# Kernel optimization log

Hardware: AMD Instinct MI355X
Metric: run time of the kernel (lower is better)

Reference implementation:

```python
import jax, jax.numpy as jnp
import numpy as np

N = 50000      # nodes
NIN = 512      # input feature dim
H = 512        # hidden width (cfg[0])
D = 128        # output embedding (cfg[1])
A = 3          # number of adjacency matrices
E = 800000     # edges per adjacency (avg degree 16)
P_DROP = 0.2


def setup_inputs() -> dict:
    key = jax.random.key(0)
    ks = jax.random.split(key, 8)
    seq_a = jax.random.normal(ks[0], (N, NIN), jnp.float32)
    # xavier-uniform-ish scaling for linear layers
    W1 = jax.random.normal(ks[1], (NIN, H), jnp.float32) * (1.0 / np.sqrt(NIN))
    b1 = jnp.zeros((H,), jnp.float32)
    W2 = jax.random.normal(ks[2], (H, D), jnp.float32) * (1.0 / np.sqrt(H))
    b2 = jnp.zeros((D,), jnp.float32)
    # COO sparse adjacencies: A matrices, E edges each; vals ~ normalized weights
    rows = jax.random.randint(ks[3], (A, E), 0, N, jnp.int32)
    cols = jax.random.randint(ks[4], (A, E), 0, N, jnp.int32)
    vals = jax.random.uniform(ks[5], (A, E), jnp.float32) * (1.0 / 16.0)
    return {"seq_a": seq_a, "W1": W1, "b1": b1, "W2": W2, "b2": b2,
            "vals": vals, "rows": rows, "cols": cols}


def _dropout(x, key, p):
    keep = jax.random.bernoulli(key, 1.0 - p, x.shape)
    return jnp.where(keep, x / (1.0 - p), jnp.zeros((), x.dtype))


def _spmm(rows_i, cols_i, vals_i, h):
    # (sparse [N,N]) @ h  via gather + segment-sum
    msg = vals_i[:, None] * h[cols_i]           # [E, D]
    return jax.ops.segment_sum(msg, rows_i, num_segments=N)


def reference(seq_a, W1, b1, W2, b2, vals, rows, cols):
    key = jax.random.key(42)
    k0, k1 = jax.random.split(key)
    # input dropout -> 2-layer MLP (Linear, ReLU, Linear)
    x = _dropout(seq_a, k0, P_DROP)
    h = jax.nn.relu(x @ W1 + b1)
    h_a = h @ W2 + b2                            # [N, D]
    h_p_0 = _dropout(h_a, k1, P_DROP)
    # per-adjacency spmm (small fixed loop over A adjacencies)
    h_p_stack = jnp.stack(
        [_spmm(rows[i], cols[i], vals[i], h_p_0) for i in range(A)])  # [A, N, D]
    h_p_fusion = jnp.mean(h_p_stack, axis=0)     # [N, D]
    return (h_a, h_p_stack, h_p_fusion)
```

## Files before the change

### kernel.cpp

```cpp
#include <hip/hip_runtime.h>
#include <stdint.h>

#define N_NODES 50000
#define M_PAD   50048
#define NIN     512
#define HDIM    512
#define DDIM    128
#define A_ADJ   3
#define E_EDGES 800000
#define TOT_E   (A_ADJ * E_EDGES)
#define TOT_ROWS (A_ADJ * N_NODES)
#define CB      49
#define NB      (A_ADJ * CB)
#define CHUNK   2048
#define NCHB    ((TOT_E + CHUNK - 1) / CHUNK)
#define TRB     640
#define DIB     25000

typedef __bf16 bf16x8 __attribute__((ext_vector_type(8)));
typedef float  f32x4  __attribute__((ext_vector_type(4)));
typedef const __attribute__((address_space(1))) void* gas1_t;
typedef __attribute__((address_space(3))) void* las3_t;

__host__ __device__ inline void tf_round(uint32_t& x0, uint32_t& x1, int r) {
  x0 += x1; x1 = (x1 << r) | (x1 >> (32 - r)); x1 ^= x0;
}
__host__ __device__ inline void threefry2x32(uint32_t k0, uint32_t k1,
                                             uint32_t x0, uint32_t x1,
                                             uint32_t& o0, uint32_t& o1) {
  uint32_t ks2 = k0 ^ k1 ^ 0x1BD11BDAu;
  x0 += k0; x1 += k1;
  tf_round(x0,x1,13); tf_round(x0,x1,15); tf_round(x0,x1,26); tf_round(x0,x1,6);
  x0 += k1; x1 += ks2 + 1u;
  tf_round(x0,x1,17); tf_round(x0,x1,29); tf_round(x0,x1,16); tf_round(x0,x1,24);
  x0 += ks2; x1 += k0 + 2u;
  tf_round(x0,x1,13); tf_round(x0,x1,15); tf_round(x0,x1,26); tf_round(x0,x1,6);
  x0 += k0; x1 += k1 + 3u;
  tf_round(x0,x1,17); tf_round(x0,x1,29); tf_round(x0,x1,16); tf_round(x0,x1,24);
  x0 += k1; x1 += ks2 + 4u;
  tf_round(x0,x1,13); tf_round(x0,x1,15); tf_round(x0,x1,26); tf_round(x0,x1,6);
  x0 += ks2; x1 += k0 + 5u;
  o0 = x0; o1 = x1;
}

__device__ inline bool keep_bit(uint32_t b) {
  float f = __uint_as_float((b >> 9) | 0x3f800000u) - 1.0f;
  return f < 0.8f;
}
__device__ inline uint16_t f2bf(float f) {
  uint32_t u = __float_as_uint(f);
  return (uint16_t)((u + 0x7fffu + ((u >> 16) & 1u)) >> 16);
}
__device__ inline float bf2f(uint16_t b) { return __uint_as_float(((uint32_t)b) << 16); }

__device__ inline uint32_t rbits32(uint32_t ka, uint32_t kb, uint32_t i) {
  uint32_t o0, o1;
  threefry2x32(ka, kb, 0u, i, o0, o1);
  return o0 ^ o1;
}

template <int MODE>
__device__ __forceinline__ void gemm_body(const uint16_t* __restrict__ A,
                                          const uint16_t* __restrict__ Bt,
                                          const float* __restrict__ bias,
                                          uint16_t* __restrict__ hOut,
                                          float* __restrict__ fOut,
                                          uint16_t* __restrict__ hp0,
                                          int Nn, int K, int bx, int by,
                                          char* smem, uint32_t ka, uint32_t kb) {
  uint16_t* As0 = (uint16_t*)smem;
  uint16_t* Bs0 = As0 + 8192;
  const int t  = threadIdx.x;
  const int w  = t >> 6, l = t & 63;
  const int lm = l & 15, kg = l >> 4;
  const int wr = w >> 1, wc = w & 1;
  const int rowbase = by * 128;
  const int colbase = bx * 128;
  const int c0 = t, c1 = t + 256;
  const int n0 = c0 >> 2, ch0 = (c0 & 3) ^ ((n0 >> 1) & 3);
  const int n1 = c1 >> 2, ch1 = (c1 & 3) ^ ((n1 >> 1) & 3);

  f32x4 acc[4][4] = {};

#define STAGEB(buf, kt)                                                             \
  {                                                                                 \
    __builtin_amdgcn_global_load_lds(                                               \
        (gas1_t)&A [(size_t)(rowbase + n0) * K + (kt) + ch0 * 8],                   \
        (las3_t)(As0 + (buf) * 4096 + c0 * 8), 16, 0, 0);                           \
    __builtin_amdgcn_global_load_lds(                                               \
        (gas1_t)&A [(size_t)(rowbase + n1) * K + (kt) + ch1 * 8],                   \
        (las3_t)(As0 + (buf) * 4096 + c1 * 8), 16, 0, 0);                           \
    __builtin_amdgcn_global_load_lds(                                               \
        (gas1_t)&Bt[(size_t)(colbase + n0) * K + (kt) + ch0 * 8],                   \
        (las3_t)(Bs0 + (buf) * 4096 + c0 * 8), 16, 0, 0);                           \
    __builtin_amdgcn_global_load_lds(                                               \
        (gas1_t)&Bt[(size_t)(colbase + n1) * K + (kt) + ch1 * 8],                   \
        (las3_t)(Bs0 + (buf) * 4096 + c1 * 8), 16, 0, 0);                           \
  }

  STAGEB(0, 0);
  asm volatile("s_waitcnt vmcnt(0)" ::: "memory");
  __syncthreads();

  const int NT = K >> 5;
  for (int tt = 0; tt < NT; ++tt) {
    const int cur = tt & 1;
    if (tt + 1 < NT) STAGEB(cur ^ 1, (tt + 1) * 32);

    const uint16_t* Asc = As0 + cur * 4096;
    const uint16_t* Bsc = Bs0 + cur * 4096;
    bf16x8 af[4], bfr[4];
#pragma unroll
    for (int m = 0; m < 4; ++m) {
      int ra = wr * 64 + m * 16 + lm;
      af[m] = *(const bf16x8*)&Asc[ra * 32 + ((kg ^ ((ra >> 1) & 3)) << 3)];
    }
#pragma unroll
    for (int n = 0; n < 4; ++n) {
      int rb = wc * 64 + n * 16 + lm;
      bfr[n] = *(const bf16x8*)&Bsc[rb * 32 + ((kg ^ ((rb >> 1) & 3)) << 3)];
    }
#pragma unroll
    for (int m = 0; m < 4; ++m)
#pragma unroll
      for (int n = 0; n < 4; ++n)
        acc[m][n] = __builtin_amdgcn_mfma_f32_16x16x32_bf16(af[m], bfr[n], acc[m][n], 0, 0, 0);

    asm volatile("s_waitcnt vmcnt(0)" ::: "memory");
    __syncthreads();
  }
#undef STAGEB

#pragma unroll
  for (int m = 0; m < 4; ++m) {
    int r0 = rowbase + wr * 64 + m * 16 + kg * 4;
#pragma unroll
    for (int n = 0; n < 4; ++n) {
      int cc = colbase + wc * 64 + n * 16 + lm;
      float bv = bias[cc];
#pragma unroll
      for (int r = 0; r < 4; ++r) {
        int row = r0 + r;
        if (row < N_NODES) {
          float v = acc[m][n][r] + bv;
          if (MODE == 0) {
            hOut[(size_t)row * Nn + cc] = f2bf(fmaxf(v, 0.0f));
          } else {
            fOut[(size_t)row * Nn + cc] = v;
            uint32_t bits = rbits32(ka, kb, (uint32_t)(row * DDIM + cc));
            hp0[(size_t)row * DDIM + cc] = f2bf(keep_bit(bits) ? v * 1.25f : 0.0f);
          }
        }
      }
    }
  }
}

struct P1S {
  uint64_t lbuf[CHUNK];
  uint16_t lbkt[CHUNK];
  uint32_t hist[NB], scn[NB], lofs[NB], base[NB];
  uint32_t hs[256];
};

__device__ __forceinline__ void pass1_body(const int* __restrict__ rows,
                                           const int* __restrict__ cols,
                                           const float* __restrict__ vals,
                                           uint32_t* __restrict__ gcur,
                                           uint64_t* __restrict__ sedgeA,
                                           int blk, char* smem) {
  P1S* S = (P1S*)smem;
  const int tid = threadIdx.x;
  const int cb = blk * CHUNK;
  const int cnt = min(CHUNK, TOT_E - cb);

  if (tid < NB) S->hist[tid] = 0;
  __syncthreads();

  uint64_t pay[8];
  uint16_t bk[8];
#pragma unroll
  for (int c = 0; c < 8; ++c) {
    int p = tid + c * 256;
    bk[c] = 0xffffu;
    if (p < cnt) {
      int e = cb + p;
      int a = e / E_EDGES;
      uint32_t r   = (uint32_t)rows[e];
      uint32_t col = (uint32_t)cols[e];
      float    v   = vals[e];
      uint16_t b = (uint16_t)(a * CB + (r >> 10));
      pay[c] = ((uint64_t)__float_as_uint(v) << 32) | ((r & 1023u) << 16) | col;
      bk[c]  = b;
      atomicAdd(&S->hist[b], 1u);
    }
  }
  __syncthreads();

  uint32_t hv = (tid < NB) ? S->hist[tid] : 0u;
  S->hs[tid] = hv;
  __syncthreads();
  for (int off = 1; off < 256; off <<= 1) {
    uint32_t v = (tid >= off) ? S->hs[tid - off] : 0u;
    __syncthreads();
    S->hs[tid] += v;
    __syncthreads();
  }
  if (tid < NB) {
    uint32_t excl = S->hs[tid] - hv;
    S->scn[tid]  = excl;
    S->lofs[tid] = excl;
    S->base[tid] = hv ? atomicAdd(&gcur[tid], hv) : 0u;
  }
  __syncthreads();

#pragma unroll
  for (int c = 0; c < 8; ++c) {
    if (bk[c] != 0xffffu) {
      uint32_t p = atomicAdd(&S->lofs[bk[c]], 1u);
      S->lbuf[p] = pay[c];
      S->lbkt[p] = bk[c];
    }
  }
  __syncthreads();

#pragma unroll
  for (int c = 0; c < 8; ++c) {
    int p = tid + c * 256;
    if (p < cnt) {
      uint16_t k = S->lbkt[p];
      sedgeA[S->base[k] + ((uint32_t)p - S->scn[k])] = S->lbuf[p];
    }
  }
}

struct P2S { uint32_t rh[1024], rs[1024], wsum[256]; };

__device__ __forceinline__ void pass2_body(const uint32_t* __restrict__ gbase,
                                           const uint64_t* __restrict__ sedgeA,
                                           uint64_t* __restrict__ sedgeB,
                                           uint32_t* __restrict__ offs,
                                           int b, char* smem) {
  P2S* S = (P2S*)smem;
  const int tid = threadIdx.x;
  const int a = b / CB, rb = (b % CB) * 1024;
  const int nrows = min(1024, N_NODES - rb);
  const uint32_t s0 = gbase[b], e0 = gbase[b + 1];

#pragma unroll
  for (int c = 0; c < 4; ++c) S->rh[tid + c * 256] = 0;
  __syncthreads();
  for (uint32_t i = s0 + tid; i < e0; i += 256) {
    uint32_t rl = ((uint32_t)(sedgeA[i] >> 16)) & 1023u;
    atomicAdd(&S->rh[rl], 1u);
  }
  __syncthreads();

  uint32_t c0 = S->rh[tid * 4], c1 = S->rh[tid * 4 + 1];
  uint32_t c2 = S->rh[tid * 4 + 2], c3 = S->rh[tid * 4 + 3];
  uint32_t tsum = c0 + c1 + c2 + c3;
  S->wsum[tid] = tsum;
  __syncthreads();
  for (int off = 1; off < 256; off <<= 1) {
    uint32_t v = (tid >= off) ? S->wsum[tid - off] : 0u;
    __syncthreads();
    S->wsum[tid] += v;
    __syncthreads();
  }
  uint32_t run = S->wsum[tid] - tsum;
  S->rs[tid * 4] = run;     run += c0;
  S->rs[tid * 4 + 1] = run; run += c1;
  S->rs[tid * 4 + 2] = run; run += c2;
  S->rs[tid * 4 + 3] = run;
  __syncthreads();

  for (int r = tid; r < 1024; r += 256) {
    if (r < nrows) offs[(size_t)a * N_NODES + rb + r] = s0 + S->rs[r];
    S->rh[r] = S->rs[r];
  }
  __syncthreads();

  for (uint32_t i = s0 + tid; i < e0; i += 256) {
    uint64_t ed = sedgeA[i];
    uint32_t rl = ((uint32_t)(ed >> 16)) & 1023u;
    uint32_t p = atomicAdd(&S->rh[rl], 1u);
    sedgeB[s0 + p] = ed;
  }
}

__global__ __launch_bounds__(256) void k_front(const float* __restrict__ W1,
                                               uint16_t* __restrict__ w1t,
                                               const float* __restrict__ W2,
                                               uint16_t* __restrict__ w2t,
                                               const float* __restrict__ seq,
                                               uint16_t* __restrict__ x,
                                               const int* __restrict__ rows,
                                               uint32_t* __restrict__ gh,
                                               uint32_t ka, uint32_t kb) {
  __shared__ uint32_t shh[NB];
  const int b = blockIdx.x, tid = threadIdx.x;
  if (b < TRB) {
    int t = b * 256 + tid;
    const int T1 = (NIN * HDIM) / 2;
    if (t < T1) {
      int k2 = (2 * t) % NIN, n = (2 * t) / NIN;
      uint32_t p = (uint32_t)f2bf(W1[(size_t)k2 * HDIM + n])
                 | ((uint32_t)f2bf(W1[(size_t)(k2 + 1) * HDIM + n]) << 16);
      *(uint32_t*)&w1t[(size_t)n * NIN + k2] = p;
    } else {
      int u = t - T1;
      int k2 = (2 * u) % HDIM, n = (2 * u) / HDIM;
      uint32_t p = (uint32_t)f2bf(W2[(size_t)k2 * DDIM + n])
                 | ((uint32_t)f2bf(W2[(size_t)(k2 + 1) * DDIM + n]) << 16);
      *(uint32_t*)&w2t[(size_t)n * HDIM + k2] = p;
    }
  } else if (b < TRB + NCHB) {
    if (tid < NB) shh[tid] = 0;
    __syncthreads();
    const int cb = (b - TRB) * CHUNK;
    const int cnt = min(CHUNK, TOT_E - cb);
    for (int c = tid; c < cnt; c += 256) {
      int e = cb + c;
      int a = e / E_EDGES;
      uint32_t r = (uint32_t)rows[e];
      atomicAdd(&shh[a * CB + (r >> 10)], 1u);
    }
    __syncthreads();
    if (tid < NB && shh[tid]) atomicAdd(&gh[tid], shh[tid]);
  } else {
    int t = (b - TRB - NCHB) * 256 + tid;
    int i0 = 4 * t;
    float4 v = ((const float4*)seq)[t];
    float f[4] = {v.x, v.y, v.z, v.w};
    uint16_t r[4];
#pragma unroll
    for (int j = 0; j < 4; ++j) {
      uint32_t bits = rbits32(ka, kb, (uint32_t)(i0 + j));
      r[j] = f2bf(keep_bit(bits) ? f[j] * 1.25f : 0.0f);
    }
    uint2 w;
    w.x = (uint32_t)r[0] | ((uint32_t)r[1] << 16);
    w.y = (uint32_t)r[2] | ((uint32_t)r[3] << 16);
    ((uint2*)x)[t] = w;
  }
}

__global__ __launch_bounds__(256) void k_bscan(const uint32_t* __restrict__ gh,
                                               uint32_t* __restrict__ gbase,
                                               uint32_t* __restrict__ gcur,
                                               uint32_t* __restrict__ offs) {
  __shared__ uint32_t s[256];
  const int tid = threadIdx.x;
  uint32_t v = (tid < NB) ? gh[tid] : 0u;
  s[tid] = v;
  __syncthreads();
  for (int off = 1; off < 256; off <<= 1) {
    uint32_t w = (tid >= off) ? s[tid - off] : 0u;
    __syncthreads();
    s[tid] += w;
    __syncthreads();
  }
  if (tid < NB) { uint32_t excl = s[tid] - v; gbase[tid] = excl; gcur[tid] = excl; }
  if (tid == NB - 1) gbase[NB] = s[tid];
  if (tid == 0) offs[TOT_ROWS] = (uint32_t)TOT_E;
}

__global__ __launch_bounds__(256) void k_mid(const uint16_t* __restrict__ x,
                                             const uint16_t* __restrict__ w1t,
                                             const float* __restrict__ b1,
                                             uint16_t* __restrict__ h,
                                             const int* __restrict__ rows,
                                             const int* __restrict__ cols,
                                             const float* __restrict__ vals,
                                             uint32_t* __restrict__ gcur,
                                             uint64_t* __restrict__ sedgeA) {
  __shared__ __align__(16) char smem[32768];
  const int b = blockIdx.x;
  if (b < 4 * (M_PAD / 128))
    gemm_body<0>(x, w1t, b1, h, nullptr, nullptr, HDIM, NIN, b & 3, b >> 2, smem, 0u, 0u);
  else
    pass1_body(rows, cols, vals, gcur, sedgeA, b - 4 * (M_PAD / 128), smem);
}

__global__ __launch_bounds__(256) void k_back(const uint16_t* __restrict__ h,
                                              const uint16_t* __restrict__ w2t,
                                              const float* __restrict__ b2,
                                              float* __restrict__ ha,
                                              uint16_t* __restrict__ hp0,
                                              const uint32_t* __restrict__ gbase,
                                              const uint64_t* __restrict__ sedgeA,
                                              uint64_t* __restrict__ sedgeB,
                                              uint32_t* __restrict__ offs,
                                              uint32_t ka, uint32_t kb) {
  __shared__ __align__(16) char smem[32768];
  const int b = blockIdx.x;
  if (b < M_PAD / 128)
    gemm_body<1>(h, w2t, b2, nullptr, ha, hp0, DDIM, HDIM, 0, b, smem, ka, kb);
  else
    pass2_body(gbase, sedgeA, sedgeB, offs, b - M_PAD / 128, smem);
}

__global__ __launch_bounds__(256) void k_spmm_csr3(const uint32_t* __restrict__ offs,
                                                   const uint64_t* __restrict__ sedge,
                                                   const uint16_t* __restrict__ hp0,
                                                   float* __restrict__ stack,
                                                   float* __restrict__ fus) {
  int row = (int)((blockIdx.x * (size_t)blockDim.x + threadIdx.x) >> 6);
  int l = threadIdx.x & 63;
  if (row >= N_NODES) return;
  const int q = l & 15, g = l >> 4;
  const uint4* hp4 = (const uint4*)hp0;
  float fs[8] = {};

#pragma unroll
  for (int a = 0; a < A_ADJ; ++a) {
    uint32_t s = offs[(size_t)a * N_NODES + row];
    uint32_t e = offs[(size_t)a * N_NODES + row + 1];
    float acc[8] = {};
    for (uint32_t i = s; i < e; i += 8) {
      uint32_t i0 = i + g, i1 = i + 4 + g;
      float v0 = 0.f, v1 = 0.f;
      uint32_t col0 = 0, col1 = 0;
      if (i0 < e) { uint64_t ed = sedge[i0]; col0 = (uint32_t)ed & 0xffffu;
                    v0 = __uint_as_float((uint32_t)(ed >> 32)); }
      if (i1 < e) { uint64_t ed = sedge[i1]; col1 = (uint32_t)ed & 0xffffu;
                    v1 = __uint_as_float((uint32_t)(ed >> 32)); }
      uint4 p0 = hp4[(size_t)col0 * 16 + q];
      uint4 p1 = hp4[(size_t)col1 * 16 + q];
      acc[0] += bf2f((uint16_t)(p0.x & 0xffffu)) * v0;  acc[1] += bf2f((uint16_t)(p0.x >> 16)) * v0;
      acc[2] += bf2f((uint16_t)(p0.y & 0xffffu)) * v0;  acc[3] += bf2f((uint16_t)(p0.y >> 16)) * v0;
      acc[4] += bf2f((uint16_t)(p0.z & 0xffffu)) * v0;  acc[5] += bf2f((uint16_t)(p0.z >> 16)) * v0;
      acc[6] += bf2f((uint16_t)(p0.w & 0xffffu)) * v0;  acc[7] += bf2f((uint16_t)(p0.w >> 16)) * v0;
      acc[0] += bf2f((uint16_t)(p1.x & 0xffffu)) * v1;  acc[1] += bf2f((uint16_t)(p1.x >> 16)) * v1;
      acc[2] += bf2f((uint16_t)(p1.y & 0xffffu)) * v1;  acc[3] += bf2f((uint16_t)(p1.y >> 16)) * v1;
      acc[4] += bf2f((uint16_t)(p1.z & 0xffffu)) * v1;  acc[5] += bf2f((uint16_t)(p1.z >> 16)) * v1;
      acc[6] += bf2f((uint16_t)(p1.w & 0xffffu)) * v1;  acc[7] += bf2f((uint16_t)(p1.w >> 16)) * v1;
    }
#pragma unroll
    for (int d = 0; d < 8; ++d) {
      acc[d] += __shfl_xor(acc[d], 16);
      acc[d] += __shfl_xor(acc[d], 32);
    }
    if (l < 16) {
      size_t b4 = ((size_t)a * N_NODES + row) * 32 + (size_t)q * 2;
      ((float4*)stack)[b4]     = make_float4(acc[0], acc[1], acc[2], acc[3]);
      ((float4*)stack)[b4 + 1] = make_float4(acc[4], acc[5], acc[6], acc[7]);
    }
#pragma unroll
    for (int d = 0; d < 8; ++d) fs[d] += acc[d];
  }
  if (l < 16) {
    const float k3 = 1.0f / 3.0f;
    size_t b4 = (size_t)row * 32 + (size_t)q * 2;
    ((float4*)fus)[b4]     = make_float4(fs[0] * k3, fs[1] * k3, fs[2] * k3, fs[3] * k3);
    ((float4*)fus)[b4 + 1] = make_float4(fs[4] * k3, fs[5] * k3, fs[6] * k3, fs[7] * k3);
  }
}

extern "C" void kernel_launch(void* const* d_in, const int* in_sizes, int n_in,
                              void* d_out, int out_size, void* d_ws, size_t ws_size,
                              hipStream_t stream) {
  const float* seq  = (const float*)d_in[0];
  const float* W1   = (const float*)d_in[1];
  const float* b1   = (const float*)d_in[2];
  const float* W2   = (const float*)d_in[3];
  const float* b2   = (const float*)d_in[4];
  const float* vals = (const float*)d_in[5];
  const int*   rows = (const int*)d_in[6];
  const int*   cols = (const int*)d_in[7];

  float* out       = (float*)d_out;
  float* out_ha    = out;
  float* out_stack = out + (size_t)N_NODES * DDIM;
  float* out_fus   = out_stack + (size_t)A_ADJ * N_NODES * DDIM;

  uint16_t* x   = (uint16_t*)d_ws;
  uint16_t* h   = x   + (size_t)M_PAD * NIN;
  uint16_t* w1t = h   + (size_t)M_PAD * HDIM;
  uint16_t* w2t = w1t + (size_t)HDIM * NIN;
  uint16_t* hp0 = w2t + (size_t)DDIM * HDIM;
  uint32_t* gh    = (uint32_t*)(hp0 + (size_t)N_NODES * DDIM);
  uint32_t* gbase = gh + 256;
  uint32_t* gcur  = gbase + 256;
  uint32_t* offs  = gcur + 256;

  uint64_t* sedgeA = (uint64_t*)out_stack;
  uint64_t* sedgeB = (uint64_t*)x;

  uint32_t k0a, k0b, k1a, k1b;
  threefry2x32(0u, 42u, 0u, 0u, k0a, k0b);
  threefry2x32(0u, 42u, 0u, 1u, k1a, k1b);

  (void)hipMemsetAsync(gh, 0, NB * sizeof(uint32_t), stream);

  k_front<<<TRB + NCHB + DIB, 256, 0, stream>>>(W1, w1t, W2, w2t, seq, x, rows, gh, k0a, k0b);

  k_bscan<<<1, 256, 0, stream>>>(gh, gbase, gcur, offs);

  k_mid<<<4 * (M_PAD / 128) + NCHB, 256, 0, stream>>>(x, w1t, b1, h, rows, cols, vals,
                                                      gcur, sedgeA);

  k_back<<<(M_PAD / 128) + NB, 256, 0, stream>>>(h, w2t, b2, out_ha, hp0,
                                                 gbase, sedgeA, sedgeB, offs, k1a, k1b);

  k_spmm_csr3<<<(N_NODES * 64 + 255) / 256, 256, 0, stream>>>(offs, sedgeB, hp0,
                                                              out_stack, out_fus);
}
```

Before: 294.2 us.

## Retile first GEMM as 64x512 full-width tiles with 512-thread blocks

The first GEMM (x @ W1) changes from 128x128 tiles over four column blocks to 64-row tiles that span the full 512-wide hidden dimension, with 8 waves per block. Each A tile is now loaded from global memory once instead of four times. The cost is more W1 traffic per block, 72KB of LDS and fewer blocks resident per CU. The co-scheduled edge-bucketing pass and k_mid are moved to 512 threads to match, and the spmm gather uses 32-bit byte offsets instead of 64-bit index math.

```diff
diff --git a/kernel.cpp b/kernel.cpp
--- a/kernel.cpp
+++ b/kernel.cpp
@@ -16,6 +16,7 @@
 #define NCHB    ((TOT_E + CHUNK - 1) / CHUNK)
 #define TRB     640
 #define DIB     25000
+#define G0B     (M_PAD / 64)
 
 typedef __bf16 bf16x8 __attribute__((ext_vector_type(8)));
 typedef float  f32x4  __attribute__((ext_vector_type(4)));
@@ -59,15 +60,88 @@
   return o0 ^ o1;
 }
 
-template <int MODE>
-__device__ __forceinline__ void gemm_body(const uint16_t* __restrict__ A,
-                                          const uint16_t* __restrict__ Bt,
-                                          const float* __restrict__ bias,
-                                          uint16_t* __restrict__ hOut,
-                                          float* __restrict__ fOut,
-                                          uint16_t* __restrict__ hp0,
-                                          int Nn, int K, int bx, int by,
-                                          char* smem, uint32_t ka, uint32_t kb) {
+__device__ __forceinline__ void gemm0_body(const uint16_t* __restrict__ x,
+                                           const uint16_t* __restrict__ w1t,
+                                           const float* __restrict__ b1,
+                                           uint16_t* __restrict__ h,
+                                           int by, char* smem) {
+  uint16_t* As0 = (uint16_t*)smem;
+  uint16_t* Bs0 = As0 + 2 * 2048;
+  const int tid = threadIdx.x;
+  const int l = tid & 63, wid = tid >> 6;
+  const int lm = l & 15, kg = l >> 4;
+  const int wrow = wid >> 2, wcol = wid & 3;
+  const int rowbase = by * 64;
+
+  f32x4 acc[2][8] = {};
+
+#define STAGE0(buf, kt)                                                             \
+  {                                                                                 \
+    if (tid < 256) {                                                                \
+      int row = tid >> 2, cs = tid & 3, ch = cs ^ ((row >> 1) & 3);                 \
+      __builtin_amdgcn_global_load_lds(                                             \
+          (gas1_t)&x[(size_t)(rowbase + row) * NIN + (kt) + ch * 8],                \
+          (las3_t)(As0 + (buf) * 2048 + tid * 8), 16, 0, 0);                        \
+    }                                                                               \
+    _Pragma("unroll")                                                               \
+    for (int it = 0; it < 4; ++it) {                                                \
+      int q = it * 512 + tid;                                                       \
+      int n = q >> 2, cs = q & 3, ch = cs ^ ((n >> 1) & 3);                         \
+      __builtin_amdgcn_global_load_lds(                                             \
+          (gas1_t)&w1t[(size_t)n * NIN + (kt) + ch * 8],                            \
+          (las3_t)(Bs0 + (buf) * 16384 + q * 8), 16, 0, 0);                         \
+    }                                                                               \
+  }
+
+  STAGE0(0, 0);
+  asm volatile("s_waitcnt vmcnt(0)" ::: "memory");
+  __syncthreads();
+
+  for (int tt = 0; tt < 16; ++tt) {
+    const int cur = tt & 1;
+    if (tt + 1 < 16) STAGE0(cur ^ 1, (tt + 1) * 32);
+
+    const uint16_t* Asc = As0 + cur * 2048;
+    const uint16_t* Bsc = Bs0 + cur * 16384;
+    const int r0a = wrow * 32 + lm, r1a = r0a + 16;
+    bf16x8 af0 = *(const bf16x8*)&Asc[r0a * 32 + ((kg ^ ((r0a >> 1) & 3)) << 3)];
+    bf16x8 af1 = *(const bf16x8*)&Asc[r1a * 32 + ((kg ^ ((r1a >> 1) & 3)) << 3)];
+#pragma unroll
+    for (int n = 0; n < 8; ++n) {
+      int rb = wcol * 128 + n * 16 + lm;
+      bf16x8 bfr = *(const bf16x8*)&Bsc[rb * 32 + ((kg ^ ((rb >> 1) & 3)) << 3)];
+      acc[0][n] = __builtin_amdgcn_mfma_f32_16x16x32_bf16(af0, bfr, acc[0][n], 0, 0, 0);
+      acc[1][n] = __builtin_amdgcn_mfma_f32_16x16x32_bf16(af1, bfr, acc[1][n], 0, 0, 0);
+    }
+    asm volatile("s_waitcnt vmcnt(0)" ::: "memory");
+    __syncthreads();
+  }
+#undef STAGE0
+
+#pragma unroll
+  for (int m = 0; m < 2; ++m) {
+    int r0 = rowbase + wrow * 32 + m * 16 + kg * 4;
+#pragma unroll
+    for (int n = 0; n < 8; ++n) {
+      int cc = wcol * 128 + n * 16 + lm;
+      float bv = b1[cc];
+#pragma unroll
+      for (int r = 0; r < 4; ++r) {
+        int row = r0 + r;
+        if (row < N_NODES)
+          h[(size_t)row * HDIM + cc] = f2bf(fmaxf(acc[m][n][r] + bv, 0.0f));
+      }
+    }
+  }
+}
+
+__device__ __forceinline__ void gemm1_body(const uint16_t* __restrict__ A,
+                                           const uint16_t* __restrict__ Bt,
+                                           const float* __restrict__ bias,
+                                           float* __restrict__ fOut,
+                                           uint16_t* __restrict__ hp0,
+                                           int by, char* smem,
+                                           uint32_t ka, uint32_t kb) {
   uint16_t* As0 = (uint16_t*)smem;
   uint16_t* Bs0 = As0 + 8192;
   const int t  = threadIdx.x;
@@ -75,14 +149,14 @@
   const int lm = l & 15, kg = l >> 4;
   const int wr = w >> 1, wc = w & 1;
   const int rowbase = by * 128;
-  const int colbase = bx * 128;
   const int c0 = t, c1 = t + 256;
   const int n0 = c0 >> 2, ch0 = (c0 & 3) ^ ((n0 >> 1) & 3);
   const int n1 = c1 >> 2, ch1 = (c1 & 3) ^ ((n1 >> 1) & 3);
+  const int K = HDIM;
 
   f32x4 acc[4][4] = {};
 
-#define STAGEB(buf, kt)                                                             \
+#define STAGE1(buf, kt)                                                             \
   {                                                                                 \
     __builtin_amdgcn_global_load_lds(                                               \
         (gas1_t)&A [(size_t)(rowbase + n0) * K + (kt) + ch0 * 8],                   \
@@ -91,21 +165,21 @@
         (gas1_t)&A [(size_t)(rowbase + n1) * K + (kt) + ch1 * 8],                   \
         (las3_t)(As0 + (buf) * 4096 + c1 * 8), 16, 0, 0);                           \
     __builtin_amdgcn_global_load_lds(                                               \
-        (gas1_t)&Bt[(size_t)(colbase + n0) * K + (kt) + ch0 * 8],                   \
+        (gas1_t)&Bt[(size_t)n0 * K + (kt) + ch0 * 8],                               \
         (las3_t)(Bs0 + (buf) * 4096 + c0 * 8), 16, 0, 0);                           \
     __builtin_amdgcn_global_load_lds(                                               \
-        (gas1_t)&Bt[(size_t)(colbase + n1) * K + (kt) + ch1 * 8],                   \
+        (gas1_t)&Bt[(size_t)n1 * K + (kt) + ch1 * 8],                               \
         (las3_t)(Bs0 + (buf) * 4096 + c1 * 8), 16, 0, 0);                           \
   }
 
-  STAGEB(0, 0);
+  STAGE1(0, 0);
   asm volatile("s_waitcnt vmcnt(0)" ::: "memory");
   __syncthreads();
 
   const int NT = K >> 5;
   for (int tt = 0; tt < NT; ++tt) {
     const int cur = tt & 1;
-    if (tt + 1 < NT) STAGEB(cur ^ 1, (tt + 1) * 32);
+    if (tt + 1 < NT) STAGE1(cur ^ 1, (tt + 1) * 32);
 
     const uint16_t* Asc = As0 + cur * 4096;
     const uint16_t* Bsc = Bs0 + cur * 4096;
@@ -129,27 +203,23 @@
     asm volatile("s_waitcnt vmcnt(0)" ::: "memory");
     __syncthreads();
   }
-#undef STAGEB
+#undef STAGE1
 
 #pragma unroll
   for (int m = 0; m < 4; ++m) {
     int r0 = rowbase + wr * 64 + m * 16 + kg * 4;
 #pragma unroll
     for (int n = 0; n < 4; ++n) {
-      int cc = colbase + wc * 64 + n * 16 + lm;
+      int cc = wc * 64 + n * 16 + lm;
       float bv = bias[cc];
 #pragma unroll
       for (int r = 0; r < 4; ++r) {
         int row = r0 + r;
         if (row < N_NODES) {
           float v = acc[m][n][r] + bv;
-          if (MODE == 0) {
-            hOut[(size_t)row * Nn + cc] = f2bf(fmaxf(v, 0.0f));
-          } else {
-            fOut[(size_t)row * Nn + cc] = v;
-            uint32_t bits = rbits32(ka, kb, (uint32_t)(row * DDIM + cc));
-            hp0[(size_t)row * DDIM + cc] = f2bf(keep_bit(bits) ? v * 1.25f : 0.0f);
-          }
+          fOut[(size_t)row * DDIM + cc] = v;
+          uint32_t bits = rbits32(ka, kb, (uint32_t)(row * DDIM + cc));
+          hp0[(size_t)row * DDIM + cc] = f2bf(keep_bit(bits) ? v * 1.25f : 0.0f);
         }
       }
     }
@@ -160,7 +230,7 @@
   uint64_t lbuf[CHUNK];
   uint16_t lbkt[CHUNK];
   uint32_t hist[NB], scn[NB], lofs[NB], base[NB];
-  uint32_t hs[256];
+  uint32_t hs[512];
 };
 
 __device__ __forceinline__ void pass1_body(const int* __restrict__ rows,
@@ -177,11 +247,11 @@
   if (tid < NB) S->hist[tid] = 0;
   __syncthreads();
 
-  uint64_t pay[8];
-  uint16_t bk[8];
-#pragma unroll
-  for (int c = 0; c < 8; ++c) {
-    int p = tid + c * 256;
+  uint64_t pay[4];
+  uint16_t bk[4];
+#pragma unroll
+  for (int c = 0; c < 4; ++c) {
+    int p = tid + c * 512;
     bk[c] = 0xffffu;
     if (p < cnt) {
       int e = cb + p;
@@ -200,7 +270,7 @@
   uint32_t hv = (tid < NB) ? S->hist[tid] : 0u;
   S->hs[tid] = hv;
   __syncthreads();
-  for (int off = 1; off < 256; off <<= 1) {
+  for (int off = 1; off < 512; off <<= 1) {
     uint32_t v = (tid >= off) ? S->hs[tid - off] : 0u;
     __syncthreads();
     S->hs[tid] += v;
@@ -215,7 +285,7 @@
   __syncthreads();
 
 #pragma unroll
-  for (int c = 0; c < 8; ++c) {
+  for (int c = 0; c < 4; ++c) {
     if (bk[c] != 0xffffu) {
       uint32_t p = atomicAdd(&S->lofs[bk[c]], 1u);
       S->lbuf[p] = pay[c];
@@ -225,8 +295,8 @@
   __syncthreads();
 
 #pragma unroll
-  for (int c = 0; c < 8; ++c) {
-    int p = tid + c * 256;
+  for (int c = 0; c < 4; ++c) {
+    int p = tid + c * 512;
     if (p < cnt) {
       uint16_t k = S->lbkt[p];
       sedgeA[S->base[k] + ((uint32_t)p - S->scn[k])] = S->lbuf[p];
@@ -365,7 +435,7 @@
   if (tid == 0) offs[TOT_ROWS] = (uint32_t)TOT_E;
 }
 
-__global__ __launch_bounds__(256) void k_mid(const uint16_t* __restrict__ x,
+__global__ __launch_bounds__(512) void k_mid(const uint16_t* __restrict__ x,
                                              const uint16_t* __restrict__ w1t,
                                              const float* __restrict__ b1,
                                              uint16_t* __restrict__ h,
@@ -374,12 +444,12 @@
                                              const float* __restrict__ vals,
                                              uint32_t* __restrict__ gcur,
                                              uint64_t* __restrict__ sedgeA) {
-  __shared__ __align__(16) char smem[32768];
+  __shared__ __align__(16) char smem[73728];
   const int b = blockIdx.x;
-  if (b < 4 * (M_PAD / 128))
-    gemm_body<0>(x, w1t, b1, h, nullptr, nullptr, HDIM, NIN, b & 3, b >> 2, smem, 0u, 0u);
+  if (b < G0B)
+    gemm0_body(x, w1t, b1, h, b, smem);
   else
-    pass1_body(rows, cols, vals, gcur, sedgeA, b - 4 * (M_PAD / 128), smem);
+    pass1_body(rows, cols, vals, gcur, sedgeA, b - G0B, smem);
 }
 
 __global__ __launch_bounds__(256) void k_back(const uint16_t* __restrict__ h,
@@ -395,7 +465,7 @@
   __shared__ __align__(16) char smem[32768];
   const int b = blockIdx.x;
   if (b < M_PAD / 128)
-    gemm_body<1>(h, w2t, b2, nullptr, ha, hp0, DDIM, HDIM, 0, b, smem, ka, kb);
+    gemm1_body(h, w2t, b2, ha, hp0, b, smem, ka, kb);
   else
     pass2_body(gbase, sedgeA, sedgeB, offs, b - M_PAD / 128, smem);
 }
@@ -409,7 +479,8 @@
   int l = threadIdx.x & 63;
   if (row >= N_NODES) return;
   const int q = l & 15, g = l >> 4;
-  const uint4* hp4 = (const uint4*)hp0;
+  const char* hpb = (const char*)hp0;
+  const uint32_t qoff = (uint32_t)(q << 4);
   float fs[8] = {};
 
 #pragma unroll
@@ -420,13 +491,13 @@
     for (uint32_t i = s; i < e; i += 8) {
       uint32_t i0 = i + g, i1 = i + 4 + g;
       float v0 = 0.f, v1 = 0.f;
-      uint32_t col0 = 0, col1 = 0;
-      if (i0 < e) { uint64_t ed = sedge[i0]; col0 = (uint32_t)ed & 0xffffu;
+      uint32_t o0 = qoff, o1 = qoff;
+      if (i0 < e) { uint64_t ed = sedge[i0]; o0 += ((uint32_t)ed & 0xffffu) << 8;
                     v0 = __uint_as_float((uint32_t)(ed >> 32)); }
-      if (i1 < e) { uint64_t ed = sedge[i1]; col1 = (uint32_t)ed & 0xffffu;
+      if (i1 < e) { uint64_t ed = sedge[i1]; o1 += ((uint32_t)ed & 0xffffu) << 8;
                     v1 = __uint_as_float((uint32_t)(ed >> 32)); }
-      uint4 p0 = hp4[(size_t)col0 * 16 + q];
-      uint4 p1 = hp4[(size_t)col1 * 16 + q];
+      uint4 p0 = *(const uint4*)(hpb + o0);
+      uint4 p1 = *(const uint4*)(hpb + o1);
       acc[0] += bf2f((uint16_t)(p0.x & 0xffffu)) * v0;  acc[1] += bf2f((uint16_t)(p0.x >> 16)) * v0;
       acc[2] += bf2f((uint16_t)(p0.y & 0xffffu)) * v0;  acc[3] += bf2f((uint16_t)(p0.y >> 16)) * v0;
       acc[4] += bf2f((uint16_t)(p0.z & 0xffffu)) * v0;  acc[5] += bf2f((uint16_t)(p0.z >> 16)) * v0;
@@ -497,8 +568,7 @@
 
   k_bscan<<<1, 256, 0, stream>>>(gh, gbase, gcur, offs);
 
-  k_mid<<<4 * (M_PAD / 128) + NCHB, 256, 0, stream>>>(x, w1t, b1, h, rows, cols, vals,
-                                                      gcur, sedgeA);
+  k_mid<<<G0B + NCHB, 512, 0, stream>>>(x, w1t, b1, h, rows, cols, vals, gcur, sedgeA);
 
   k_back<<<(M_PAD / 128) + NB, 256, 0, stream>>>(h, w2t, b2, out_ha, hp0,
                                                  gbase, sedgeA, sedgeB, offs, k1a, k1b);
```

New measurement: 314.0 us. 6.7% more time.
